# Performance work log

Measured on AMD Instinct MI355X. Metric: run time of the kernel, lower is better.

Reference implementation:

```python
import jax, jax.numpy as jnp
import numpy as np

E, H, KVH, S, N = 2048, 16, 4, 4096, 1
D = E // H            # head_dim = 128
G = H // KVH          # groups = 4
KV_DIM = KVH * D


def setup_inputs() -> dict:
    key = jax.random.key(0)
    ks = jax.random.split(key, 7)
    sc = 0.02
    seq = jax.random.normal(ks[0], (N, S, E), dtype=jnp.float32)
    # causal mask, 0 = masked (matches masked_fill(mask == 0, -inf))
    mask = jnp.tril(jnp.ones((S, S), dtype=jnp.int32))[None, None]  # [1,1,S,S]
    return {
        "seq": seq,
        "mask": mask,
        "Wq_w": jax.random.normal(ks[1], (E, E), dtype=jnp.float32) * sc,
        "Wq_b": jnp.zeros((E,), dtype=jnp.float32),
        "Wkv_w": jax.random.normal(ks[2], (2 * KV_DIM, E), dtype=jnp.float32) * sc,
        "Wkv_b": jnp.zeros((2 * KV_DIM,), dtype=jnp.float32),
        "Wo_w": jax.random.normal(ks[3], (E, E), dtype=jnp.float32) * sc,
        "Wo_b": jnp.zeros((E,), dtype=jnp.float32),
    }


def reference(seq, mask, Wq_w, Wq_b, Wkv_w, Wkv_b, Wo_w, Wo_b):
    n, s, _ = seq.shape
    q = seq @ Wq_w.T + Wq_b                      # [N,S,E]
    kv = seq @ Wkv_w.T + Wkv_b                   # [N,S,2*KV_DIM]
    Q = q.reshape(n, s, H, D).transpose(0, 2, 1, 3)         # [N,H,S,D]
    KV = kv.reshape(n, s, 2, KVH, D)
    K = KV[:, :, 0].transpose(0, 2, 1, 3)                   # [N,KVH,S,D]
    V = KV[:, :, 1].transpose(0, 2, 1, 3)                   # [N,KVH,S,D]
    # repeat_interleave over head dim (GQA expansion)
    Kr = jnp.repeat(K, G, axis=1)                           # [N,H,S,D]
    Vr = jnp.repeat(V, G, axis=1)
    energy = jnp.einsum("nhqd,nhkd->nhqk", Q, Kr)           # [N,H,S,S]
    neg = jnp.finfo(energy.dtype).min
    energy = jnp.where(mask == 0, neg, energy)
    attn = jax.nn.softmax(energy / jnp.sqrt(jnp.float32(D)), axis=3)
    out = jnp.einsum("nhqk,nhkd->nhqd", attn, Vr)           # [N,H,S,D]
    out = out.transpose(0, 2, 1, 3).reshape(n, s, E)
    out = out @ Wo_w.T + Wo_b
    return out, K, V
```

## Files before the change

kernel.cpp:

```cpp
#include <hip/hip_runtime.h>
#include <cstdint>
#include <cstddef>

typedef __bf16 bf16_t;
typedef __bf16 bf16x4 __attribute__((ext_vector_type(4)));
typedef __bf16 bf16x8 __attribute__((ext_vector_type(8)));
typedef float  f32x4  __attribute__((ext_vector_type(4)));

#define LDQ 3072

__global__ __launch_bounds__(256)
void cast_kernel(const float* __restrict__ in, bf16_t* __restrict__ out, int n8) {
  int i = blockIdx.x * 256 + threadIdx.x;
  if (i >= n8) return;
  const float4* p = reinterpret_cast<const float4*>(in) + (size_t)i * 2;
  float4 a = p[0], b = p[1];
  bf16x8 o;
  o[0] = (bf16_t)a.x; o[1] = (bf16_t)a.y; o[2] = (bf16_t)a.z; o[3] = (bf16_t)a.w;
  o[4] = (bf16_t)b.x; o[5] = (bf16_t)b.y; o[6] = (bf16_t)b.z; o[7] = (bf16_t)b.w;
  *reinterpret_cast<bf16x8*>(out + (size_t)i * 8) = o;
}

template <int MODE>
__global__ __launch_bounds__(512, 2)
void gemm256(const bf16_t* __restrict__ A, const bf16_t* __restrict__ B,
             const float* __restrict__ bias0, const float* __restrict__ bias1,
             void* __restrict__ out0, float* __restrict__ kvout,
             bf16_t* __restrict__ vt, int M, int N, int K) {
  __shared__ __align__(16) char smem[65536];
  const int t = threadIdx.x;
  const int l = t & 63;
  const int lr = l & 15, lh = l >> 4;
  const int w = t >> 6;
  const int wm = w >> 2, wn = w & 3;
  const int m0 = blockIdx.x * 256, n0 = blockIdx.y * 256;

  const char* Ag = (const char*)(A + (size_t)m0 * K);
  const char* Bg = (const char*)(B + (size_t)n0 * K);

#define STAGE_U(dst, src, ks)                                                   \
  { _Pragma("unroll")                                                           \
    for (int p = 0; p < 2; ++p) {                                               \
      int c = p * 512 + t;                                                      \
      int row = c >> 2;                                                         \
      int c16 = (c & 3) ^ ((row >> 1) & 3);                                     \
      __builtin_amdgcn_global_load_lds(                                         \
        (const __attribute__((address_space(1))) void*)                         \
          ((src) + (size_t)row * (size_t)(K * 2) + (size_t)(ks) * 64 + c16 * 16), \
        (__attribute__((address_space(3))) void*)((dst) + c * 16), 16, 0, 0);   \
    } }

  f32x4 acc[8][4] = {};
  bf16x8 a[4], b[4];
  char* const s0 = smem;
  char* const s1 = smem + 32768;

#define RD_B(base)                                                              \
  { _Pragma("unroll")                                                           \
    for (int j = 0; j < 4; ++j) {                                               \
      int row = wn * 64 + j * 16 + lr;                                          \
      b[j] = *reinterpret_cast<const bf16x8*>(                                  \
          (base) + 16384 + row * 64 + ((lh ^ ((row >> 1) & 3)) << 4));          \
    } }
#define RD_A(base, iq)                                                          \
  { _Pragma("unroll")                                                           \
    for (int i = 0; i < 4; ++i) {                                               \
      int row = wm * 128 + (iq) * 64 + i * 16 + lr;                             \
      a[i] = *reinterpret_cast<const bf16x8*>(                                  \
          (base) + row * 64 + ((lh ^ ((row >> 1) & 3)) << 4));                  \
    } }
#define MFMA16(iq)                                                              \
  asm volatile("s_waitcnt lgkmcnt(0)" ::: "memory");                            \
  __builtin_amdgcn_sched_barrier(0);                                            \
  __builtin_amdgcn_s_setprio(1);                                                \
  { _Pragma("unroll")                                                           \
    for (int i = 0; i < 4; ++i)                                                 \
      _Pragma("unroll")                                                         \
      for (int j = 0; j < 4; ++j)                                               \
        acc[(iq) * 4 + i][j] =                                                  \
          __builtin_amdgcn_mfma_f32_16x16x32_bf16(a[i], b[j], acc[(iq)*4+i][j], 0, 0, 0); } \
  __builtin_amdgcn_s_setprio(0);                                                \
  __builtin_amdgcn_sched_barrier(0);
#define BAR  __builtin_amdgcn_s_barrier(); __builtin_amdgcn_sched_barrier(0);

  const int NK = K >> 5;
  STAGE_U(s0, Ag, 0);
  STAGE_U(s0 + 16384, Bg, 0);

  for (int it2 = 0; it2 < (NK >> 1); ++it2) {
    const int k1 = 2 * it2 + 1, k2 = 2 * it2 + 2;
    STAGE_U(s1, Ag, k1);
    asm volatile("s_waitcnt vmcnt(2)" ::: "memory");
    BAR;
    RD_B(s0); RD_A(s0, 0);
    MFMA16(0);
    BAR;
    RD_A(s0, 1);
    STAGE_U(s1 + 16384, Bg, k1);
    MFMA16(1);
    BAR;
    if (k2 < NK) {
      STAGE_U(s0, Ag, k2);
      asm volatile("s_waitcnt vmcnt(2)" ::: "memory");
    } else {
      asm volatile("s_waitcnt vmcnt(0)" ::: "memory");
    }
    BAR;
    RD_B(s1); RD_A(s1, 0);
    MFMA16(0);
    BAR;
    RD_A(s1, 1);
    if (k2 < NK) STAGE_U(s0 + 16384, Bg, k2);
    MFMA16(1);
    BAR;
  }
#undef STAGE_U
#undef RD_A
#undef RD_B
#undef MFMA16
#undef BAR

  #pragma unroll
  for (int j = 0; j < 4; ++j) {
    const int col = n0 + wn * 64 + j * 16 + lr;
    float bv;
    if constexpr (MODE == 0) bv = bias0[col];
    else bv = (col < 2048) ? bias0[col] : bias1[col - 2048];
    #pragma unroll
    for (int i = 0; i < 8; ++i) {
      #pragma unroll
      for (int r = 0; r < 4; ++r) {
        const int row = m0 + wm * 128 + i * 16 + lh * 4 + r;
        float v = acc[i][j][r] + bv;
        if constexpr (MODE == 0) {
          reinterpret_cast<float*>(out0)[(size_t)row * N + col] = v;
        } else {
          float qv = (col < 2048) ? v * 0.1275187541f : v;
          reinterpret_cast<bf16_t*>(out0)[(size_t)row * N + col] = (bf16_t)qv;
          if (col >= 2048) {
            const int local = col - 2048;
            const int which = local >> 9;
            const int hd    = local & 511;
            kvout[(size_t)which * 2097152 +
                  ((size_t)(hd >> 7) * 4096 + row) * 128 + (hd & 127)] = v;
            if (local >= 512) {
              const int c2 = local - 512;
              vt[(size_t)(c2 >> 7) * 524288 + (size_t)(c2 & 127) * 4096 + row] = (bf16_t)v;
            }
          }
        }
      }
    }
  }
}

__global__ __launch_bounds__(512, 2)
void attn_kernel(const bf16_t* __restrict__ QKVb, const bf16_t* __restrict__ Vt,
                 bf16_t* __restrict__ Ob) {
  __shared__ __align__(16) char smem[65536];
  const int t = threadIdx.x;
  const int w = t >> 6, l = t & 63;
  const int lr = l & 15, lh = l >> 4;
  const int g = w >> 2;
  const int wq = w & 3;
  const int h = blockIdx.y, kvh = h >> 2;

  const char* Kg = (const char*)(QKVb + 2048 + (size_t)kvh * 128);
  const char* Vg = (const char*)(Vt + (size_t)kvh * 524288);

#define STAGE_K(buf, kv0)                                                          \
  {                                                                                \
    _Pragma("unroll")                                                              \
    for (int p = 0; p < 2; ++p) {                                                  \
      int chunk = p * 512 + t;                                                     \
      int row = chunk >> 4, cb = (chunk & 15) << 4;                                \
      __builtin_amdgcn_global_load_lds(                                            \
        (const __attribute__((address_space(1))) void*)                            \
            (Kg + (size_t)((kv0) + row) * 6144 + (cb ^ ((row & 7) << 4))),         \
        (__attribute__((address_space(3))) void*)(smem + (buf) * 16384 + chunk * 16),\
        16, 0, 0);                                                                 \
    }                                                                              \
  }
#define STAGE_V(buf, kv0)                                                          \
  {                                                                                \
    _Pragma("unroll")                                                              \
    for (int p = 0; p < 2; ++p) {                                                  \
      int chunk = p * 512 + t;                                                     \
      int row = chunk >> 3, cb = (chunk & 7) << 4;                                 \
      __builtin_amdgcn_global_load_lds(                                            \
        (const __attribute__((address_space(1))) void*)                            \
            (Vg + (size_t)row * 8192 + (size_t)(kv0) * 2 + (cb ^ ((row & 7) << 4))),\
        (__attribute__((address_space(3))) void*)(smem + 32768 + (buf) * 16384 + chunk * 16),\
        16, 0, 0);                                                                 \
    }                                                                              \
  }

  bf16x8 onesf;
  #pragma unroll
  for (int j = 0; j < 8; ++j) onesf[j] = (bf16_t)1.0f;

  for (int ph = 0; ph < 2; ++ph) {
    const int xt = ph ? 31 - (int)blockIdx.x : (int)blockIdx.x;
    const int q0b = xt * 128;
    const int q0w = q0b + wq * 32;
    const int nIter = 2 * xt + 2;

    bf16x8 qf[2][4];
    #pragma unroll
    for (int sub = 0; sub < 2; ++sub) {
      const bf16_t* qp = QKVb + (size_t)(q0w + sub * 16 + lr) * LDQ + h * 128 + lh * 8;
      #pragma unroll
      for (int kc = 0; kc < 4; ++kc) qf[sub][kc] = *reinterpret_cast<const bf16x8*>(qp + kc * 32);
    }
    __builtin_amdgcn_sched_barrier(0);
    STAGE_K(0, 0);
    STAGE_V(0, 0);
    __builtin_amdgcn_sched_barrier(0);
    STAGE_K(1, 64);
    STAGE_V(1, 64);
    __builtin_amdgcn_sched_barrier(0);

    f32x4 oacc[2][8] = {};
    f32x4 lacc[2] = {};

    auto body = [&](int it, bool masked) {
      const int cur = it & 1;
      const int kv0 = it * 64;
      if (it + 1 < nIter) { asm volatile("s_waitcnt vmcnt(4)" ::: "memory"); }
      else                { asm volatile("s_waitcnt vmcnt(0)" ::: "memory"); }
      __builtin_amdgcn_s_barrier();
      __builtin_amdgcn_sched_barrier(0);

      const char* kb = smem + cur * 16384;
      f32x4 s[2][2] = {};
      __builtin_amdgcn_s_setprio(1);
      #pragma unroll
      for (int n2 = 0; n2 < 2; ++n2) {
        const int row = g * 32 + n2 * 16 + lr;
        const int sw = (row & 7) << 4;
        #pragma unroll
        for (int kc = 0; kc < 4; ++kc) {
          bf16x8 kf = *reinterpret_cast<const bf16x8*>(kb + row * 256 + ((kc * 64 + lh * 16) ^ sw));
          s[0][n2] = __builtin_amdgcn_mfma_f32_16x16x32_bf16(kf, qf[0][kc], s[0][n2], 0, 0, 0);
          s[1][n2] = __builtin_amdgcn_mfma_f32_16x16x32_bf16(kf, qf[1][kc], s[1][n2], 0, 0, 0);
        }
      }
      __builtin_amdgcn_s_setprio(0);

      bf16x8 pa[2];
      #pragma unroll
      for (int sub = 0; sub < 2; ++sub) {
        const int qs = q0w + sub * 16;
        const bool needM = masked && (kv0 + g * 32 + 31 > qs);
        bf16x8 v;
        #pragma unroll
        for (int n2 = 0; n2 < 2; ++n2) {
          #pragma unroll
          for (int r = 0; r < 4; ++r) {
            float p = exp2f(s[sub][n2][r]);
            if (needM && (kv0 + g * 32 + n2 * 16 + lh * 4 + r > qs + lr)) p = 0.f;
            v[n2 * 4 + r] = (bf16_t)p;
          }
        }
        pa[sub] = v;
      }
      lacc[0] = __builtin_amdgcn_mfma_f32_16x16x32_bf16(pa[0], onesf, lacc[0], 0, 0, 0);
      lacc[1] = __builtin_amdgcn_mfma_f32_16x16x32_bf16(pa[1], onesf, lacc[1], 0, 0, 0);

      const char* vb0 = smem + 32768 + cur * 16384;
      __builtin_amdgcn_s_setprio(1);
      #pragma unroll
      for (int nb = 0; nb < 8; ++nb) {
        const int row = nb * 16 + lr;
        const int sw2 = (row & 7) << 4;
        const char* vb = vb0 + row * 128;
        bf16x4 lo = *reinterpret_cast<const bf16x4*>(vb + ((g * 64 + lh * 8) ^ sw2));
        bf16x4 hi = *reinterpret_cast<const bf16x4*>(vb + ((g * 64 + 32 + lh * 8) ^ sw2));
        bf16x8 vf = __builtin_shufflevector(lo, hi, 0, 1, 2, 3, 4, 5, 6, 7);
        oacc[0][nb] = __builtin_amdgcn_mfma_f32_16x16x32_bf16(pa[0], vf, oacc[0][nb], 0, 0, 0);
        oacc[1][nb] = __builtin_amdgcn_mfma_f32_16x16x32_bf16(pa[1], vf, oacc[1][nb], 0, 0, 0);
      }
      __builtin_amdgcn_s_setprio(0);

      __builtin_amdgcn_sched_barrier(0);
      __builtin_amdgcn_s_barrier();
      __builtin_amdgcn_sched_barrier(0);
      if (it + 2 < nIter) { STAGE_K(cur, kv0 + 128); STAGE_V(cur, kv0 + 128); }
    };

    for (int it = 0; it < nIter - 2; ++it) body(it, false);
    body(nIter - 2, true);
    body(nIter - 1, true);

    bf16_t* mO = (bf16_t*)smem;
    float*  mL = (float*)(smem + 32768);
    if (g == 1) {
      #pragma unroll
      for (int sub = 0; sub < 2; ++sub) {
        #pragma unroll
        for (int nb = 0; nb < 8; ++nb)
          #pragma unroll
          for (int r = 0; r < 4; ++r)
            mO[((wq * 32 + sub * 16 + lh * 4 + r) << 7) + nb * 16 + lr] = (bf16_t)oacc[sub][nb][r];
        if (lr == 0)
          #pragma unroll
          for (int r = 0; r < 4; ++r) mL[wq * 32 + sub * 16 + lh * 4 + r] = lacc[sub][r];
      }
    }
    __syncthreads();
    if (g == 0) {
      #pragma unroll
      for (int sub = 0; sub < 2; ++sub) {
        f32x4 linv;
        #pragma unroll
        for (int r = 0; r < 4; ++r)
          linv[r] = 1.0f / (lacc[sub][r] + mL[wq * 32 + sub * 16 + lh * 4 + r]);
        #pragma unroll
        for (int nb = 0; nb < 8; ++nb) {
          #pragma unroll
          for (int r = 0; r < 4; ++r) {
            float o1 = (float)mO[((wq * 32 + sub * 16 + lh * 4 + r) << 7) + nb * 16 + lr];
            float v = (oacc[sub][nb][r] + o1) * linv[r];
            Ob[(size_t)(q0w + sub * 16 + lh * 4 + r) * 2048 + h * 128 + nb * 16 + lr] = (bf16_t)v;
          }
        }
      }
    }
    __syncthreads();
  }
#undef STAGE_K
#undef STAGE_V
}

extern "C" void kernel_launch(void* const* d_in, const int* in_sizes, int n_in,
                              void* d_out, int out_size, void* d_ws, size_t ws_size,
                              hipStream_t stream) {
  const float* seq   = (const float*)d_in[0];
  const float* Wq_w  = (const float*)d_in[2];
  const float* Wq_b  = (const float*)d_in[3];
  const float* Wkv_w = (const float*)d_in[4];
  const float* Wkv_b = (const float*)d_in[5];
  const float* Wo_w  = (const float*)d_in[6];
  const float* Wo_b  = (const float*)d_in[7];

  float* out   = (float*)d_out;
  float* kvout = out + (size_t)4096 * 2048;

  char* ws = (char*)d_ws;
  bf16_t* seqb = (bf16_t*)ws;
  bf16_t* wqkv = (bf16_t*)(ws + 16777216);
  bf16_t* wob  = (bf16_t*)(ws + 29360128);
  bf16_t* qkvb = (bf16_t*)(ws + 37748736);
  bf16_t* vt   = (bf16_t*)(ws + 62914560);
  bf16_t* ob   = seqb;

  cast_kernel<<<4096, 256, 0, stream>>>(seq, seqb, 1048576);
  cast_kernel<<<2048, 256, 0, stream>>>(Wq_w, wqkv, 524288);
  cast_kernel<<<1024, 256, 0, stream>>>(Wkv_w, wqkv + 4194304, 262144);
  cast_kernel<<<2048, 256, 0, stream>>>(Wo_w, wob, 524288);

  gemm256<1><<<dim3(16, 12), 512, 0, stream>>>(seqb, wqkv, Wq_b, Wkv_b,
                                               qkvb, kvout, vt, 4096, 3072, 2048);
  attn_kernel<<<dim3(16, 16), 512, 0, stream>>>(qkvb, vt, ob);
  gemm256<0><<<dim3(16, 8), 512, 0, stream>>>(ob, wob, Wo_b, nullptr,
                                              out, nullptr, nullptr, 4096, 2048, 2048);
}
```

Baseline: 266.3 us.

## Shrink GEMM and attention tiles to raise block count on the GPU

Replaces the 256x256 GEMM tile with 512 threads by a 128x128 tile with 256 threads, quadrupling the grid, and halves the attention query tile from 128 to 64 rows with 256 threads, doubling its grid. The aim is to fill all compute units: the previous grids of 192, 128 and 256 blocks underfill the device. In exchange, each block reuses less data per load, so global and LDS traffic per FLOP rises and barriers are amortised over less math. In the attention kernel the causal masking now applies only to the last KV iteration.

```diff
diff --git a/kernel.cpp b/kernel.cpp
--- a/kernel.cpp
+++ b/kernel.cpp
@@ -22,18 +22,18 @@
 }
 
 template <int MODE>
-__global__ __launch_bounds__(512, 2)
-void gemm256(const bf16_t* __restrict__ A, const bf16_t* __restrict__ B,
+__global__ __launch_bounds__(256, 3)
+void gemm128(const bf16_t* __restrict__ A, const bf16_t* __restrict__ B,
              const float* __restrict__ bias0, const float* __restrict__ bias1,
              void* __restrict__ out0, float* __restrict__ kvout,
              bf16_t* __restrict__ vt, int M, int N, int K) {
-  __shared__ __align__(16) char smem[65536];
+  __shared__ __align__(16) char smem[32768];
   const int t = threadIdx.x;
   const int l = t & 63;
   const int lr = l & 15, lh = l >> 4;
   const int w = t >> 6;
-  const int wm = w >> 2, wn = w & 3;
-  const int m0 = blockIdx.x * 256, n0 = blockIdx.y * 256;
+  const int wm = w >> 1, wn = w & 1;
+  const int m0 = blockIdx.x * 128, n0 = blockIdx.y * 128;
 
   const char* Ag = (const char*)(A + (size_t)m0 * K);
   const char* Bg = (const char*)(B + (size_t)n0 * K);
@@ -41,7 +41,7 @@
 #define STAGE_U(dst, src, ks)                                                   \
   { _Pragma("unroll")                                                           \
     for (int p = 0; p < 2; ++p) {                                               \
-      int c = p * 512 + t;                                                      \
+      int c = p * 256 + t;                                                      \
       int row = c >> 2;                                                         \
       int c16 = (c & 3) ^ ((row >> 1) & 3);                                     \
       __builtin_amdgcn_global_load_lds(                                         \
@@ -50,54 +50,54 @@
         (__attribute__((address_space(3))) void*)((dst) + c * 16), 16, 0, 0);   \
     } }
 
-  f32x4 acc[8][4] = {};
+  f32x4 acc[4][4] = {};
   bf16x8 a[4], b[4];
   char* const s0 = smem;
-  char* const s1 = smem + 32768;
+  char* const s1 = smem + 16384;
 
 #define RD_B(base)                                                              \
   { _Pragma("unroll")                                                           \
     for (int j = 0; j < 4; ++j) {                                               \
       int row = wn * 64 + j * 16 + lr;                                          \
       b[j] = *reinterpret_cast<const bf16x8*>(                                  \
-          (base) + 16384 + row * 64 + ((lh ^ ((row >> 1) & 3)) << 4));          \
+          (base) + 8192 + row * 64 + ((lh ^ ((row >> 1) & 3)) << 4));           \
     } }
-#define RD_A(base, iq)                                                          \
+#define RD_A2(base, i0)                                                         \
   { _Pragma("unroll")                                                           \
-    for (int i = 0; i < 4; ++i) {                                               \
-      int row = wm * 128 + (iq) * 64 + i * 16 + lr;                             \
-      a[i] = *reinterpret_cast<const bf16x8*>(                                  \
+    for (int ii = 0; ii < 2; ++ii) {                                            \
+      int row = wm * 64 + ((i0) + ii) * 16 + lr;                                \
+      a[(i0) + ii] = *reinterpret_cast<const bf16x8*>(                          \
           (base) + row * 64 + ((lh ^ ((row >> 1) & 3)) << 4));                  \
     } }
-#define MFMA16(iq)                                                              \
+#define MFMA8(i0)                                                               \
   asm volatile("s_waitcnt lgkmcnt(0)" ::: "memory");                            \
   __builtin_amdgcn_sched_barrier(0);                                            \
   __builtin_amdgcn_s_setprio(1);                                                \
   { _Pragma("unroll")                                                           \
-    for (int i = 0; i < 4; ++i)                                                 \
+    for (int ii = 0; ii < 2; ++ii)                                              \
       _Pragma("unroll")                                                         \
       for (int j = 0; j < 4; ++j)                                               \
-        acc[(iq) * 4 + i][j] =                                                  \
-          __builtin_amdgcn_mfma_f32_16x16x32_bf16(a[i], b[j], acc[(iq)*4+i][j], 0, 0, 0); } \
+        acc[(i0) + ii][j] =                                                     \
+          __builtin_amdgcn_mfma_f32_16x16x32_bf16(a[(i0)+ii], b[j], acc[(i0)+ii][j], 0, 0, 0); } \
   __builtin_amdgcn_s_setprio(0);                                                \
   __builtin_amdgcn_sched_barrier(0);
 #define BAR  __builtin_amdgcn_s_barrier(); __builtin_amdgcn_sched_barrier(0);
 
   const int NK = K >> 5;
   STAGE_U(s0, Ag, 0);
-  STAGE_U(s0 + 16384, Bg, 0);
+  STAGE_U(s0 + 8192, Bg, 0);
 
   for (int it2 = 0; it2 < (NK >> 1); ++it2) {
     const int k1 = 2 * it2 + 1, k2 = 2 * it2 + 2;
     STAGE_U(s1, Ag, k1);
     asm volatile("s_waitcnt vmcnt(2)" ::: "memory");
     BAR;
-    RD_B(s0); RD_A(s0, 0);
-    MFMA16(0);
-    BAR;
-    RD_A(s0, 1);
-    STAGE_U(s1 + 16384, Bg, k1);
-    MFMA16(1);
+    RD_B(s0); RD_A2(s0, 0);
+    MFMA8(0);
+    BAR;
+    RD_A2(s0, 2);
+    STAGE_U(s1 + 8192, Bg, k1);
+    MFMA8(2);
     BAR;
     if (k2 < NK) {
       STAGE_U(s0, Ag, k2);
@@ -106,18 +106,18 @@
       asm volatile("s_waitcnt vmcnt(0)" ::: "memory");
     }
     BAR;
-    RD_B(s1); RD_A(s1, 0);
-    MFMA16(0);
-    BAR;
-    RD_A(s1, 1);
-    if (k2 < NK) STAGE_U(s0 + 16384, Bg, k2);
-    MFMA16(1);
+    RD_B(s1); RD_A2(s1, 0);
+    MFMA8(0);
+    BAR;
+    RD_A2(s1, 2);
+    if (k2 < NK) STAGE_U(s0 + 8192, Bg, k2);
+    MFMA8(2);
     BAR;
   }
 #undef STAGE_U
-#undef RD_A
+#undef RD_A2
 #undef RD_B
-#undef MFMA16
+#undef MFMA8
 #undef BAR
 
   #pragma unroll
@@ -127,10 +127,10 @@
     if constexpr (MODE == 0) bv = bias0[col];
     else bv = (col < 2048) ? bias0[col] : bias1[col - 2048];
     #pragma unroll
-    for (int i = 0; i < 8; ++i) {
+    for (int i = 0; i < 4; ++i) {
       #pragma unroll
       for (int r = 0; r < 4; ++r) {
-        const int row = m0 + wm * 128 + i * 16 + lh * 4 + r;
+        const int row = m0 + wm * 64 + i * 16 + lh * 4 + r;
         float v = acc[i][j][r] + bv;
         if constexpr (MODE == 0) {
           reinterpret_cast<float*>(out0)[(size_t)row * N + col] = v;
@@ -154,15 +154,15 @@
   }
 }
 
-__global__ __launch_bounds__(512, 2)
+__global__ __launch_bounds__(256, 2)
 void attn_kernel(const bf16_t* __restrict__ QKVb, const bf16_t* __restrict__ Vt,
                  bf16_t* __restrict__ Ob) {
   __shared__ __align__(16) char smem[65536];
   const int t = threadIdx.x;
   const int w = t >> 6, l = t & 63;
   const int lr = l & 15, lh = l >> 4;
-  const int g = w >> 2;
-  const int wq = w & 3;
+  const int g = w >> 1;
+  const int wq = w & 1;
   const int h = blockIdx.y, kvh = h >> 2;
 
   const char* Kg = (const char*)(QKVb + 2048 + (size_t)kvh * 128);
@@ -171,8 +171,8 @@
 #define STAGE_K(buf, kv0)                                                          \
   {                                                                                \
     _Pragma("unroll")                                                              \
-    for (int p = 0; p < 2; ++p) {                                                  \
-      int chunk = p * 512 + t;                                                     \
+    for (int p = 0; p < 4; ++p) {                                                  \
+      int chunk = p * 256 + t;                                                     \
       int row = chunk >> 4, cb = (chunk & 15) << 4;                                \
       __builtin_amdgcn_global_load_lds(                                            \
         (const __attribute__((address_space(1))) void*)                            \
@@ -184,8 +184,8 @@
 #define STAGE_V(buf, kv0)                                                          \
   {                                                                                \
     _Pragma("unroll")                                                              \
-    for (int p = 0; p < 2; ++p) {                                                  \
-      int chunk = p * 512 + t;                                                     \
+    for (int p = 0; p < 4; ++p) {                                                  \
+      int chunk = p * 256 + t;                                                     \
       int row = chunk >> 3, cb = (chunk & 7) << 4;                                 \
       __builtin_amdgcn_global_load_lds(                                            \
         (const __attribute__((address_space(1))) void*)                            \
@@ -200,10 +200,10 @@
   for (int j = 0; j < 8; ++j) onesf[j] = (bf16_t)1.0f;
 
   for (int ph = 0; ph < 2; ++ph) {
-    const int xt = ph ? 31 - (int)blockIdx.x : (int)blockIdx.x;
-    const int q0b = xt * 128;
+    const int xt = ph ? 63 - (int)blockIdx.x : (int)blockIdx.x;
+    const int q0b = xt * 64;
     const int q0w = q0b + wq * 32;
-    const int nIter = 2 * xt + 2;
+    const int nIter = xt + 1;
 
     bf16x8 qf[2][4];
     #pragma unroll
@@ -226,7 +226,7 @@
     auto body = [&](int it, bool masked) {
       const int cur = it & 1;
       const int kv0 = it * 64;
-      if (it + 1 < nIter) { asm volatile("s_waitcnt vmcnt(4)" ::: "memory"); }
+      if (it + 1 < nIter) { asm volatile("s_waitcnt vmcnt(8)" ::: "memory"); }
       else                { asm volatile("s_waitcnt vmcnt(0)" ::: "memory"); }
       __builtin_amdgcn_s_barrier();
       __builtin_amdgcn_sched_barrier(0);
@@ -288,8 +288,7 @@
       if (it + 2 < nIter) { STAGE_K(cur, kv0 + 128); STAGE_V(cur, kv0 + 128); }
     };
 
-    for (int it = 0; it < nIter - 2; ++it) body(it, false);
-    body(nIter - 2, true);
+    for (int it = 0; it < nIter - 1; ++it) body(it, false);
     body(nIter - 1, true);
 
     bf16_t* mO = (bf16_t*)smem;
@@ -359,9 +358,9 @@
   cast_kernel<<<1024, 256, 0, stream>>>(Wkv_w, wqkv + 4194304, 262144);
   cast_kernel<<<2048, 256, 0, stream>>>(Wo_w, wob, 524288);
 
-  gemm256<1><<<dim3(16, 12), 512, 0, stream>>>(seqb, wqkv, Wq_b, Wkv_b,
+  gemm128<1><<<dim3(32, 24), 256, 0, stream>>>(seqb, wqkv, Wq_b, Wkv_b,
                                                qkvb, kvout, vt, 4096, 3072, 2048);
-  attn_kernel<<<dim3(16, 16), 512, 0, stream>>>(qkvb, vt, ob);
-  gemm256<0><<<dim3(16, 8), 512, 0, stream>>>(ob, wob, Wo_b, nullptr,
-                                              out, nullptr, nullptr, 4096, 2048, 2048);
+  attn_kernel<<<dim3(32, 16), 256, 0, stream>>>(qkvb, vt, ob);
+  gemm128<0><<<dim3(32, 16), 256, 0, stream>>>(ob, wob, Wo_b, nullptr,
+                                               out, nullptr, nullptr, 4096, 2048, 2048);
 }
```

New measurement: 225.2 us. -15.4%, faster.
